# Kernel tuning notes

Measured on AMD Instinct MI355X. Metric: run time of the kernel, lower is better.

The kernel has to match this reference:

```python
import jax, jax.numpy as jnp
import numpy as np

B, P, C = 256, 196, 512       # batch, num_pixels, encoder_dim
D, A, E = 512, 256, 256       # decoder_dim, attention_dim, embedding_dim
V, TC = 193, 256              # vocab, caption length (decode steps = TC-1)


def _lin(k, out_d, in_d):
    s = 1.0 / np.sqrt(in_d)
    return jax.random.uniform(k, (out_d, in_d), jnp.float32, -s, s)


def setup_inputs() -> dict:
    key = jax.random.key(0)
    ks = jax.random.split(key, 16)
    lens = jax.random.randint(ks[1], (B,), 2, TC + 1).at[0].set(TC)
    inp = {
        "encoder_output": jax.random.normal(ks[0], (B, P, C), jnp.float32),
        "encoded_captions": jax.random.randint(ks[2], (B, TC), 0, V),
        "caption_lengths": lens[:, None],
        # attention
        "W_enc_att": _lin(ks[3], A, C), "b_enc_att": jnp.zeros((A,), jnp.float32),
        "W_dec_att": _lin(ks[4], A, D), "b_dec_att": jnp.zeros((A,), jnp.float32),
        "W_full_att": _lin(ks[5], 1, A), "b_full_att": jnp.zeros((1,), jnp.float32),
        # embedding (init uniform(-0.1, 0.1) as in init_weigths)
        "embedding": jax.random.uniform(ks[6], (V, E), jnp.float32, -0.1, 0.1),
        # output projection
        "W_fc": jax.random.uniform(ks[7], (V, D), jnp.float32, -0.1, 0.1),
        "b_fc": jnp.zeros((V,), jnp.float32),
        # LSTMCell: input is [emb ; attended_enc] -> E + C
        "W_ih": _lin(ks[8], 4 * D, E + C), "b_ih": jnp.zeros((4 * D,), jnp.float32),
        "W_hh": _lin(ks[9], 4 * D, D), "b_hh": jnp.zeros((4 * D,), jnp.float32),
        # hidden/cell init + gate
        "W_init_h": _lin(ks[10], D, C), "b_init_h": jnp.zeros((D,), jnp.float32),
        "W_init_c": _lin(ks[11], D, C), "b_init_c": jnp.zeros((D,), jnp.float32),
        "W_fbeta": _lin(ks[12], D, C), "b_fbeta": jnp.zeros((D,), jnp.float32),
    }
    return inp


def reference(encoder_output, encoded_captions, caption_lengths,
              W_enc_att, b_enc_att, W_dec_att, b_dec_att, W_full_att, b_full_att,
              embedding, W_fc, b_fc, W_ih, b_ih, W_hh, b_hh,
              W_init_h, b_init_h, W_init_c, b_init_c, W_fbeta, b_fbeta):
    b = encoder_output.shape[0]
    enc = encoder_output.reshape(b, -1, encoder_output.shape[-1])  # [B,P,C]
    lens = caption_lengths[:, 0]
    sort_index = jnp.argsort(-lens)                 # descending length sort
    lens = lens[sort_index]
    enc = enc[sort_index]
    caps = encoded_captions[sort_index]
    decode_lengths = lens - 1
    T = caps.shape[1] - 1                           # static max decode steps

    embs = embedding[caps]                          # [B,TC,E]
    mean_enc = enc.mean(axis=1)                     # [B,C]
    h0 = mean_enc @ W_init_h.T + b_init_h
    c0 = mean_enc @ W_init_c.T + b_init_c

    enc_att = enc @ W_enc_att.T + b_enc_att         # [B,P,A] precomputed
    wf, bf = W_full_att[0], b_full_att[0]

    def step(carry, xs):
        h, c = carry
        emb_t, t = xs
        # soft attention
        dec_att = h @ W_dec_att.T + b_dec_att                       # [B,A]
        scores = jnp.einsum('bpa,a->bp',
                            jax.nn.relu(enc_att + dec_att[:, None, :]), wf) + bf
        alpha = jax.nn.softmax(scores, axis=1)                      # [B,P]
        awe = jnp.einsum('bpc,bp->bc', enc, alpha)                  # [B,C]
        gate = jax.nn.sigmoid(h @ W_fbeta.T + b_fbeta)              # [B,D]
        awe = gate * awe
        # LSTM cell (torch gate order: i,f,g,o); dropout is identity in eval
        x = jnp.concatenate([emb_t, awe], axis=1)                   # [B,E+C]
        gates = x @ W_ih.T + b_ih + h @ W_hh.T + b_hh
        i_g, f_g, g_g, o_g = jnp.split(gates, 4, axis=1)
        c_new = jax.nn.sigmoid(f_g) * c + jax.nn.sigmoid(i_g) * jnp.tanh(g_g)
        h_new = jax.nn.sigmoid(o_g) * jnp.tanh(c_new)
        # shrinking-batch semantics: inactive rows keep state, emit zeros
        active = (t < decode_lengths)[:, None]
        h2 = jnp.where(active, h_new, h)
        c2 = jnp.where(active, c_new, c)
        preds = jnp.where(active, h_new @ W_fc.T + b_fc, 0.0)
        alpha = jnp.where(active, alpha, 0.0)
        return (h2, c2), (preds, alpha)

    xs = (jnp.swapaxes(embs[:, :T], 0, 1), jnp.arange(T))
    _, (preds, alphas) = jax.lax.scan(step, (h0, c0), xs)
    predictions = jnp.swapaxes(preds, 0, 1)   # [B,T,V]
    alphas = jnp.swapaxes(alphas, 0, 1)       # [B,T,P]
    return predictions, caps, decode_lengths, alphas, sort_index
```

## Files before the change

kernel.cpp:

```cpp
#include <hip/hip_runtime.h>
#include <cstdint>
#include <cstddef>


typedef unsigned short u16;
typedef unsigned int u32;
typedef unsigned long long ull;
typedef __attribute__((ext_vector_type(8))) short short8;
typedef __attribute__((ext_vector_type(4))) float f32x4;

__device__ __forceinline__ float sigf(float x){ return 1.f/(1.f+expf(-x)); }
__device__ __forceinline__ u16 f2bf(float f){
  u32 u = __builtin_bit_cast(u32, f);
  u32 r = (u + 0x7fffu + ((u>>16)&1u)) >> 16;
  return (u16)r;
}
__device__ __forceinline__ float bf2f(u16 u){
  u32 x = ((u32)u) << 16;
  return __builtin_bit_cast(float, x);
}

__device__ __forceinline__ void st_dev_f32(float* p, float v){
  __hip_atomic_store(p, v, __ATOMIC_RELAXED, __HIP_MEMORY_SCOPE_AGENT);
}
__device__ __forceinline__ float ld_dev_f32(const float* p){
  return __hip_atomic_load(p, __ATOMIC_RELAXED, __HIP_MEMORY_SCOPE_AGENT);
}
__device__ __forceinline__ void st_dev_u16(u16* p, u16 v){
  __hip_atomic_store(p, v, __ATOMIC_RELAXED, __HIP_MEMORY_SCOPE_AGENT);
}
__device__ __forceinline__ void st_dev_u32(u32* p, u32 v){
  __hip_atomic_store(p, v, __ATOMIC_RELAXED, __HIP_MEMORY_SCOPE_AGENT);
}
__device__ __forceinline__ u32 ld_dev_u32(const u32* p){
  return __hip_atomic_load(p, __ATOMIC_RELAXED, __HIP_MEMORY_SCOPE_AGENT);
}
__device__ __forceinline__ ull ld_dev_u64(const ull* p){
  return __hip_atomic_load(p, __ATOMIC_RELAXED, __HIP_MEMORY_SCOPE_AGENT);
}

__device__ __forceinline__ void ctr_signal(int* c){
  __syncthreads();
  if (threadIdx.x == 0)
    __hip_atomic_fetch_add(c, 1, __ATOMIC_RELAXED, __HIP_MEMORY_SCOPE_AGENT);
}
__device__ __forceinline__ void ctr_wait(int* c, int target){
  if (threadIdx.x == 0){
    int spins = 0;
    while (__hip_atomic_load(c, __ATOMIC_RELAXED, __HIP_MEMORY_SCOPE_AGENT) < target){
      if (++spins > (1<<20)) break;
      __builtin_amdgcn_s_sleep(4);
    }
  }
  __syncthreads();
}

__global__ void k_zero(float* a, int na4, float* b, int nb4, int* ctr){
  int i = blockIdx.x*blockDim.x + threadIdx.x;
  int stride = gridDim.x*blockDim.x;
  float4 z = make_float4(0.f,0.f,0.f,0.f);
  for (int j = i; j < na4; j += stride) ((float4*)a)[j] = z;
  for (int j = i; j < nb4; j += stride) ((float4*)b)[j] = z;
  if (i < 512) ctr[i] = 0;
}

__global__ void k_sort(const int* cap_lens, int* si, int* dlw, float* out_dl, float* out_si){
  __shared__ int lens[256];
  int tid = threadIdx.x;
  lens[tid] = cap_lens[tid];
  __syncthreads();
  int L = lens[tid];
  int rank = 0;
  for (int j = 0; j < 256; ++j){
    int Lj = lens[j];
    rank += ((Lj > L) || (Lj == L && j < tid)) ? 1 : 0;
  }
  si[rank] = tid;
  dlw[rank] = L - 1;
  out_dl[rank] = (float)(L - 1);
  out_si[rank] = (float)tid;
}

__global__ void k_caps(const int* caps, const int* si, int* caps_s, float* out_caps){
  int b = blockIdx.x, t = threadIdx.x;
  int v = caps[si[b]*256 + t];
  caps_s[b*256 + t] = v;
  out_caps[b*256 + t] = (float)v;
}

__global__ void k_prep(const float* enc, const int* si, u16* enc_sb){
  int b = blockIdx.x, tid = threadIdx.x;
  const float* src = enc + (size_t)si[b]*100352;
  u16* dst = enc_sb + (size_t)b*100352;
  for (int i = tid; i < 25088; i += 256){
    float4 v = *(const float4*)&src[i*4];
    ushort4 o;
    o.x = f2bf(v.x); o.y = f2bf(v.y); o.z = f2bf(v.z); o.w = f2bf(v.w);
    *(ushort4*)&dst[i*4] = o;
  }
}

__global__ void k_mean(const float* enc, const int* si, u16* mean_bf){
  int b = blockIdx.x, tid = threadIdx.x;
  const float* eb = enc + (size_t)si[b]*100352;
  int cc = 2*tid;
  float s0 = 0.f, s1 = 0.f;
  #pragma unroll 4
  for (int pp = 0; pp < 196; ++pp){
    float2 v = *(const float2*)&eb[(size_t)pp*512 + cc];
    s0 += v.x; s1 += v.y;
  }
  mean_bf[b*512 + cc]     = f2bf(s0 * (1.f/196.f));
  mean_bf[b*512 + cc + 1] = f2bf(s1 * (1.f/196.f));
}

struct ConcatP {
  const float *Wdec,*bdec,*Wfb,*bfb,*Wfc,*bfc,*Wih,*bih,*Whh,*bhh,*Winh,*binh,*Winc,*binc,*Wenc,*emb;
  u16 *Wc0,*Wc1,*Wc3,*Wenc_bf,*emb_bf;
  float *bc0,*bc1,*bc3;
};
__global__ void k_concat(ConcatP p){
  int idx = blockIdx.x*blockDim.x + threadIdx.x;
  int stride = gridDim.x*blockDim.x;
  for (int i = idx; i < 1024*512; i += stride){
    int n = i >> 9, k = i & 511;
    float v = (n < 512) ? p.Winh[n*512 + k] : p.Winc[(n-512)*512 + k];
    p.Wc0[i] = f2bf(v);
  }
  for (int i = idx; i < 1024; i += stride)
    p.bc0[i] = (i < 512) ? p.binh[i] : p.binc[i-512];
  for (int i = idx; i < 1024*512; i += stride){
    int n = i >> 9, k = i & 511;
    float v = (n < 256) ? p.Wdec[n*512+k]
            : (n < 768) ? p.Wfb[(n-256)*512+k]
            : (n < 961) ? p.Wfc[(n-768)*512+k] : 0.f;
    p.Wc1[i] = f2bf(v);
  }
  for (int i = idx; i < 1024; i += stride)
    p.bc1[i] = (i < 256) ? p.bdec[i] : (i < 768) ? p.bfb[i-256] : (i < 961) ? p.bfc[i-768] : 0.f;
  for (int i = idx; i < 2048*1280; i += stride){
    int n = i / 1280, k = i - n*1280;
    int j = n >> 2, g = n & 3, orow = g*512 + j;
    float v = (k < 768) ? p.Wih[orow*768 + k] : p.Whh[orow*512 + (k - 768)];
    p.Wc3[i] = f2bf(v);
  }
  for (int i = idx; i < 2048; i += stride){
    int j = i >> 2, g = i & 3, orow = g*512 + j;
    p.bc3[i] = p.bih[orow] + p.bhh[orow];
  }
  for (int i = idx; i < 256*512; i += stride) p.Wenc_bf[i] = f2bf(p.Wenc[i]);
  for (int i = idx; i < 193*256; i += stride) p.emb_bf[i] = f2bf(p.emb[i]);
}

struct MfmaP {
  const u16* A; const u16* Bw; const float* bias;
  int K, N;
  u16* out_bf;
  u16* h_bf; float* c;
};

template<int MODE, int NT>
__global__ __launch_bounds__(256) void k_mfma(MfmaP p){
  __shared__ __align__(16) unsigned char smem[16384 + 16384*NT];
  u16* As0 = (u16*)smem;
  u16* Bs0 = (u16*)(smem + 16384);

  const int tid  = threadIdx.x;
  const int bn0  = blockIdx.x * 64 * NT;
  const int bm0  = blockIdx.y * 64;
  const int wave = tid >> 6;
  const int lane = tid & 63;
  const int ln   = lane & 15;
  const int quad = lane >> 4;

  f32x4 acc[4][NT] = {};
  short8 pa[2], pb[2*NT];

  const int srow = tid >> 3;
  const int sgc  = tid & 7;

  #pragma unroll
  for (int r = 0; r < 2; ++r)
    pa[r] = *(const short8*)(p.A + (size_t)(bm0 + srow + 32*r)*p.K + sgc*8);
  #pragma unroll
  for (int r = 0; r < 2*NT; ++r)
    pb[r] = *(const short8*)(p.Bw + (size_t)(bn0 + srow + 32*r)*p.K + sgc*8);
  #pragma unroll
  for (int r = 0; r < 2; ++r){
    int row = srow + 32*r;
    *(short8*)&As0[row*64 + ((sgc ^ (row & 7))<<3)] = pa[r];
  }
  #pragma unroll
  for (int r = 0; r < 2*NT; ++r){
    int row = srow + 32*r;
    *(short8*)&Bs0[row*64 + ((sgc ^ (row & 7))<<3)] = pb[r];
  }

  const int nIter = p.K >> 6;
  int ib = 0;
  for (int it = 0; ; ){
    __syncthreads();
    const bool more = (it + 1 < nIter);
    if (more){
      int k0 = (it + 1) << 6;
      #pragma unroll
      for (int r = 0; r < 2; ++r)
        pa[r] = *(const short8*)(p.A + (size_t)(bm0 + srow + 32*r)*p.K + k0 + sgc*8);
      #pragma unroll
      for (int r = 0; r < 2*NT; ++r)
        pb[r] = *(const short8*)(p.Bw + (size_t)(bn0 + srow + 32*r)*p.K + k0 + sgc*8);
    }
    const u16* As = &As0[ib*4096];
    const u16* Bs = &Bs0[ib*4096*NT];
    #pragma unroll
    for (int kk = 0; kk < 2; ++kk){
      short8 af[4], bfr[NT];
      #pragma unroll
      for (int mt = 0; mt < 4; ++mt){
        int row = mt*16 + ln;
        int g = kk*4 + quad;
        af[mt] = *(const short8*)&As[row*64 + ((g ^ (row & 7))<<3)];
      }
      #pragma unroll
      for (int nt = 0; nt < NT; ++nt){
        int row = (wave*NT + nt)*16 + ln;
        int g = kk*4 + quad;
        bfr[nt] = *(const short8*)&Bs[row*64 + ((g ^ (row & 7))<<3)];
      }
      #pragma unroll
      for (int mt = 0; mt < 4; ++mt)
        #pragma unroll
        for (int nt = 0; nt < NT; ++nt)
          acc[mt][nt] = __builtin_amdgcn_mfma_f32_16x16x32_bf16(af[mt], bfr[nt], acc[mt][nt], 0, 0, 0);
    }
    if (!more) break;
    ib ^= 1;
    u16* Aw = &As0[ib*4096];
    u16* Bww = &Bs0[ib*4096*NT];
    #pragma unroll
    for (int r = 0; r < 2; ++r){
      int row = srow + 32*r;
      *(short8*)&Aw[row*64 + ((sgc ^ (row & 7))<<3)] = pa[r];
    }
    #pragma unroll
    for (int r = 0; r < 2*NT; ++r){
      int row = srow + 32*r;
      *(short8*)&Bww[row*64 + ((sgc ^ (row & 7))<<3)] = pb[r];
    }
    ++it;
  }

  #pragma unroll
  for (int nt = 0; nt < NT; ++nt){
    int n = bn0 + (wave*NT + nt)*16 + ln;
    float bv = p.bias[n];
    #pragma unroll
    for (int mt = 0; mt < 4; ++mt)
      #pragma unroll
      for (int r = 0; r < 4; ++r){
        int m = bm0 + mt*16 + quad*4 + r;
        float v = acc[mt][nt][r] + bv;
        if (MODE == 0){
          p.out_bf[(size_t)m*p.N + n] = f2bf(v);
        } else {
          if (n < 512) p.h_bf[m*512 + n] = f2bf(v);
          else         p.c[m*512 + n - 512] = v;
        }
      }
  }
}

struct PersistP {
  const u16* Wc1; const float* bc1;
  const u16* Wc3; const float* bc3;
  u16* h_bf; float* c; u16* z_bf;
  float* dec_att; float* gatev; float* preds; float* alphas;
  const u16* enc_att; const u16* enc_sb;
  const float* wfull; const float* bfull;
  const u16* emb_bf; const int* caps_s;
  const int* dl;
  int* ctr;
};

template<int NC, int MODE>
__device__ void gemm_phase(const PersistP& p, unsigned char* smem, int bm0, int bn0, int t){
  constexpr int K = NC * 64;
  constexpr int DP = (NC < 4) ? NC : 4;
  const u16* A    = (MODE == 2) ? p.h_bf : p.z_bf;
  const u16* Bw   = (MODE == 2) ? p.Wc1  : p.Wc3;
  const float* bias = (MODE == 2) ? p.bc1 : p.bc3;

  const int tid = threadIdx.x;
  const int w = tid >> 6, l = tid & 63;
  const int half = tid >> 9;
  const int loc = tid & 511;
  const int r = loc >> 3, g = loc & 7;
  u16* lds0 = (u16*)smem;
  u16* ldst = lds0 + (half ? 4096 : 0) + r*64 + ((g ^ (r & 7)) << 3);
  const u16* gp = half ? (Bw + (size_t)(bn0 + r)*K + g*8)
                       : (A  + (size_t)(bm0 + r)*K + g*8);
  const int mt = w >> 2, nt = w & 3;
  const int ln = l & 15, quad = l >> 4;
  f32x4 acc = {0.f,0.f,0.f,0.f};

  ull buf[DP][2];
  auto issue = [&](int ci, int slot){
    const u16* q = gp + ci*64;
    if (half == 0){
      buf[slot][0] = ld_dev_u64((const ull*)q);
      buf[slot][1] = ld_dev_u64((const ull*)q + 1);
    } else {
      buf[slot][0] = ((const ull*)q)[0];
      buf[slot][1] = ((const ull*)q)[1];
    }
  };
  auto wr = [&](int ci, int slot){
    u16* d = ldst + (ci & 1)*8192;
    ((ull*)d)[0] = buf[slot][0];
    ((ull*)d)[1] = buf[slot][1];
  };
  auto compute = [&](int ci){
    const u16* As = lds0 + (ci & 1)*8192;
    const u16* Bs = As + 4096;
    #pragma unroll
    for (int kk = 0; kk < 2; ++kk){
      int gg = kk*4 + quad;
      int ra = mt*16 + ln;
      short8 af = *(const short8*)&As[ra*64 + ((gg ^ (ra & 7))<<3)];
      int rb = nt*16 + ln;
      short8 bv = *(const short8*)&Bs[rb*64 + ((gg ^ (rb & 7))<<3)];
      acc = __builtin_amdgcn_mfma_f32_16x16x32_bf16(af, bv, acc, 0, 0, 0);
    }
  };

  #pragma unroll
  for (int s = 0; s < DP; ++s) issue(s, s);
  wr(0, 0);
  asm volatile("s_waitcnt lgkmcnt(0)" ::: "memory");
  __builtin_amdgcn_s_barrier();
  #pragma unroll
  for (int ci = 0; ci < NC; ++ci){
    if (ci + 1 < NC) wr(ci + 1, (ci + 1) % DP);
    if (ci + DP < NC) issue(ci + DP, (ci + DP) % DP);
    compute(ci);
    asm volatile("s_waitcnt lgkmcnt(0)" ::: "memory");
    __builtin_amdgcn_s_barrier();
  }

  if (MODE == 2){
    const int n = bn0 + nt*16 + ln;
    const float bv = bias[n];
    #pragma unroll
    for (int rr = 0; rr < 4; ++rr){
      int m = bm0 + mt*16 + quad*4 + rr;
      float v = acc[rr] + bv;
      if (n < 256)      st_dev_f32(&p.dec_att[m*256 + n], v);
      else if (n < 768) st_dev_f32(&p.gatev[m*512 + n - 256], sigf(v));
      else if (n < 961){
        int tp = t - 1;
        if (tp >= 0)
          p.preds[((size_t)m*255 + tp)*193 + (n - 768)] = (tp < p.dl[m]) ? v : 0.f;
      }
    }
  } else {
    float* Cs = (float*)smem;
    const int n_loc = nt*16 + ln;
    const float bv = bias[bn0 + n_loc];
    __syncthreads();
    #pragma unroll
    for (int rr = 0; rr < 4; ++rr)
      Cs[(mt*16 + quad*4 + rr)*68 + n_loc] = acc[rr] + bv;
    __syncthreads();
    {
      int m = tid >> 4, jl = tid & 15;
      float4 g4 = *(const float4*)&Cs[m*68 + jl*4];
      int gm = bm0 + m;
      int gj = (bn0 >> 2) + jl;
      if (t < p.dl[gm]){
        float ig = sigf(g4.x), fg = sigf(g4.y);
        float gg = tanhf(g4.z), og = sigf(g4.w);
        float cn = fg * p.c[gm*512 + gj] + ig * gg;
        float hn = og * tanhf(cn);
        p.c[gm*512 + gj] = cn;
        st_dev_u16(&p.h_bf[gm*512 + gj], f2bf(hn));
      }
    }
  }
}

__device__ void attn_phase(const PersistP& p, unsigned char* smem_raw, int b, int t){
  float* da  = (float*)smem_raw;
  float* wfs = da + 256;
  float* sc  = wfs + 256;
  float* awe = sc + 256;
  float* red = awe + 2048;
  const int tid = threadIdx.x;
  if (tid < 256){
    da[tid]  = ld_dev_f32(&p.dec_att[b*256 + tid]);
    wfs[tid] = p.wfull[tid];
  }
  __syncthreads();

  {
    const int pr = tid >> 2, aq = tid & 3;
    float s = 0.f;
    if (pr < 196){
      const u16* row = p.enc_att + ((size_t)b*196 + pr)*256 + aq*64;
      const float* dd = &da[aq*64];
      const float* ww = &wfs[aq*64];
      #pragma unroll
      for (int i = 0; i < 8; ++i){
        short8 v = *(const short8*)(row + i*8);
        #pragma unroll
        for (int j = 0; j < 8; ++j)
          s += fmaxf(bf2f((u16)v[j]) + dd[i*8+j], 0.f) * ww[i*8+j];
      }
    }
    s += __shfl_xor(s, 1, 64);
    s += __shfl_xor(s, 2, 64);
    if ((tid & 3) == 0 && pr < 196) sc[pr] = s + p.bfull[0];
  }
  __syncthreads();

  const int wid = tid >> 6, lane = tid & 63;
  float sv = (tid < 196) ? sc[tid] : -1e30f;
  float mx = sv;
  for (int o = 32; o > 0; o >>= 1) mx = fmaxf(mx, __shfl_down(mx, o, 64));
  if (lane == 0) red[wid] = mx;
  __syncthreads();
  if (tid == 0) red[16] = fmaxf(fmaxf(red[0], red[1]), fmaxf(red[2], red[3]));
  __syncthreads();
  mx = red[16];
  float e = (tid < 196) ? expf(sv - mx) : 0.f;
  float sm = e;
  for (int o = 32; o > 0; o >>= 1) sm += __shfl_down(sm, o, 64);
  if (lane == 0) red[wid] = sm;
  __syncthreads();
  if (tid == 0) red[16] = red[0] + red[1] + red[2] + red[3];
  __syncthreads();
  const float inv = 1.f / red[16];
  if (tid < 256) sc[tid] = e * inv;
  __syncthreads();
  if (tid < 196)
    p.alphas[((size_t)b*255 + t)*196 + tid] = sc[tid];

  {
    const int q = tid >> 8, cp = tid & 255, cc = 2*cp;
    const u16* eb = p.enc_sb + (size_t)b*100352;
    const int p0 = q*49;
    float v0 = 0.f, v1 = 0.f;
    #pragma unroll 7
    for (int i = 0; i < 49; ++i){
      int pp = p0 + i;
      u32 u = *(const u32*)&eb[(size_t)pp*512 + cc];
      float a = sc[pp];
      v0 += a * bf2f((u16)(u & 0xffffu));
      v1 += a * bf2f((u16)(u >> 16));
    }
    *(float2*)&awe[q*512 + cc] = make_float2(v0, v1);
  }
  __syncthreads();

  if (tid < 256){
    const int cc = 2*tid;
    float v0 = awe[0*512+cc]   + awe[1*512+cc]   + awe[2*512+cc]   + awe[3*512+cc];
    float v1 = awe[0*512+cc+1] + awe[1*512+cc+1] + awe[2*512+cc+1] + awe[3*512+cc+1];
    u16* zb = p.z_bf + (size_t)b*1280;
    float g0 = ld_dev_f32(&p.gatev[b*512 + cc]);
    float g1 = ld_dev_f32(&p.gatev[b*512 + cc + 1]);
    st_dev_u16(&zb[256 + cc],     f2bf(g0 * v0));
    st_dev_u16(&zb[256 + cc + 1], f2bf(g1 * v1));
    int tok = p.caps_s[b*256 + t];
    st_dev_u16(&zb[tid], p.emb_bf[tok*256 + tid]);
    st_dev_u32((u32*)&zb[768 + cc], ld_dev_u32((const u32*)&p.h_bf[b*512 + cc]));
  }
}

__global__ __launch_bounds__(1024) void k_persist(PersistP p){
  __shared__ __align__(16) unsigned char smem[40960];
  const int b = blockIdx.x;
  for (int t = 0; t <= 255; ++t){
    if (b >= 192){
      const int idx = b - 192, x = idx & 15, y = idx >> 4;
      ctr_wait(p.ctr + 256 + y*32, 32*t);
      if (p.dl[y*64] >= t)
        gemm_phase<8,2>(p, smem, y*64, x*64, t);
      ctr_signal(p.ctr + 0 + y*32);
    }
    if (t == 255) break;
    {
      const int y = b >> 6;
      ctr_wait(p.ctr + 0 + y*32, 16*(t+1));
      if (t < p.dl[b]) attn_phase(p, smem, b, t);
      ctr_signal(p.ctr + 128 + y*32);
    }
    if (b < 128){
      const int x = b & 31, y = b >> 5;
      ctr_wait(p.ctr + 128 + y*32, 64*(t+1));
      if (p.dl[y*64] > t)
        gemm_phase<20,3>(p, smem, y*64, x*64, t);
      ctr_signal(p.ctr + 256 + y*32);
    }
  }
}

extern "C" void kernel_launch(void* const* d_in, const int* in_sizes, int n_in,
                              void* d_out, int out_size, void* d_ws, size_t ws_size,
                              hipStream_t stream){
  (void)in_sizes; (void)n_in; (void)out_size; (void)ws_size;
  const float* enc   = (const float*)d_in[0];
  const int*   caps  = (const int*)d_in[1];
  const int*   clens = (const int*)d_in[2];
  const float* Wenc  = (const float*)d_in[3];
  const float* benc  = (const float*)d_in[4];
  const float* Wdec  = (const float*)d_in[5];
  const float* bdec  = (const float*)d_in[6];
  const float* Wfull = (const float*)d_in[7];
  const float* bfull = (const float*)d_in[8];
  const float* emb   = (const float*)d_in[9];
  const float* Wfc   = (const float*)d_in[10];
  const float* bfc   = (const float*)d_in[11];
  const float* Wih   = (const float*)d_in[12];
  const float* bih   = (const float*)d_in[13];
  const float* Whh   = (const float*)d_in[14];
  const float* bhh   = (const float*)d_in[15];
  const float* Winh  = (const float*)d_in[16];
  const float* binh  = (const float*)d_in[17];
  const float* Winc  = (const float*)d_in[18];
  const float* binc  = (const float*)d_in[19];
  const float* Wfb   = (const float*)d_in[20];
  const float* bfb   = (const float*)d_in[21];

  float* out       = (float*)d_out;
  float* out_preds = out;
  float* out_caps  = out + 12599040;
  float* out_dl    = out + 12664576;
  float* out_alph  = out + 12664832;
  float* out_si    = out + 25459712;

  char* w = (char*)d_ws;
  size_t off = 0;
  auto alloc = [&](size_t bytes) -> void* {
    void* pp = w + off; off += (bytes + 255) & ~(size_t)255; return pp;
  };
  int*   si      = (int*)  alloc(256*4);
  int*   dlw     = (int*)  alloc(256*4);
  int*   caps_s  = (int*)  alloc(65536*4);
  float* c       = (float*)alloc(131072*4);
  float* dec_att = (float*)alloc(65536*4);
  float* gatev   = (float*)alloc(131072*4);
  float* bc0     = (float*)alloc(1024*4);
  float* bc1     = (float*)alloc(1024*4);
  float* bc3     = (float*)alloc(2048*4);
  int*   ctr     = (int*)  alloc(1024*4);
  u16*   mean_bf = (u16*)  alloc(131072*2);
  u16*   h_bf    = (u16*)  alloc(131072*2);
  u16*   z_bf    = (u16*)  alloc(327680*2);
  u16*   Wc0     = (u16*)  alloc(524288*2);
  u16*   Wc1     = (u16*)  alloc(524288*2);
  u16*   Wc3     = (u16*)  alloc(2621440*2);
  u16*   Wenc_bf = (u16*)  alloc(131072*2);
  u16*   emb_bf  = (u16*)  alloc(49408*2);
  u16*   enc_sb  = (u16*)  alloc(25690112ull*2);
  u16*   enc_att = (u16*)  alloc(12845056ull*2);

  k_zero<<<1024, 256, 0, stream>>>(out_preds, 12599040/4, out_alph, 12794880/4, ctr);
  k_sort<<<1, 256, 0, stream>>>(clens, si, dlw, out_dl, out_si);
  k_caps<<<256, 256, 0, stream>>>(caps, si, caps_s, out_caps);
  k_prep<<<256, 256, 0, stream>>>(enc, si, enc_sb);
  k_mean<<<256, 256, 0, stream>>>(enc, si, mean_bf);
  ConcatP cp{Wdec,bdec,Wfb,bfb,Wfc,bfc,Wih,bih,Whh,bhh,Winh,binh,Winc,binc,Wenc,emb,
             Wc0,Wc1,Wc3,Wenc_bf,emb_bf,bc0,bc1,bc3};
  k_concat<<<2048, 256, 0, stream>>>(cp);

  {
    MfmaP g{};
    g.A = mean_bf; g.Bw = Wc0; g.bias = bc0; g.K = 512; g.N = 1024;
    g.h_bf = h_bf; g.c = c;
    k_mfma<1,1><<<dim3(16,4), 256, 0, stream>>>(g);
  }
  {
    MfmaP g{};
    g.A = enc_sb; g.Bw = Wenc_bf; g.bias = benc; g.K = 512; g.N = 256;
    g.out_bf = enc_att;
    k_mfma<0,2><<<dim3(2,784), 256, 0, stream>>>(g);
  }

  PersistP pp{};
  pp.Wc1 = Wc1; pp.bc1 = bc1; pp.Wc3 = Wc3; pp.bc3 = bc3;
  pp.h_bf = h_bf; pp.c = c; pp.z_bf = z_bf;
  pp.dec_att = dec_att; pp.gatev = gatev; pp.preds = out_preds; pp.alphas = out_alph;
  pp.enc_att = enc_att; pp.enc_sb = enc_sb;
  pp.wfull = Wfull; pp.bfull = bfull;
  pp.emb_bf = emb_bf; pp.caps_s = caps_s;
  pp.dl = dlw; pp.ctr = ctr;

  void* kargs[] = { (void*)&pp };
  hipError_t e = hipLaunchCooperativeKernel((const void*)k_persist, dim3(256), dim3(1024),
                                            kargs, 0, stream);
  if (e != hipSuccess){
    k_persist<<<dim3(256), dim3(1024), 0, stream>>>(pp);
  }
}
```

Measured before the change: 8.351 ms.

## Replace atomic counters with per-block flags and finer-grained dependency waits

Swaps the shared atomic-increment counters between persistent phases for per-producer flag slots that each block stores with the step number. Waiters poll all flags with one wavefront using a wave-wide all-reduce. The attention phase now waits only on the first four gate-GEMM tiles (the dec_att columns) before starting, and waits on the remaining gate tiles just before it needs gatev. This cuts atomic contention and overlaps attention work with the rest of that GEMM, but it depends on the tile-to-column mapping being right and on the inactive-row paths still storing their flags.

```diff
diff --git a/kernel.cpp b/kernel.cpp
--- a/kernel.cpp
+++ b/kernel.cpp
@@ -39,17 +39,21 @@
   return __hip_atomic_load(p, __ATOMIC_RELAXED, __HIP_MEMORY_SCOPE_AGENT);
 }
 
-__device__ __forceinline__ void ctr_signal(int* c){
+__device__ __forceinline__ void flag_store(int* f, int v){
   __syncthreads();
   if (threadIdx.x == 0)
-    __hip_atomic_fetch_add(c, 1, __ATOMIC_RELAXED, __HIP_MEMORY_SCOPE_AGENT);
-}
-__device__ __forceinline__ void ctr_wait(int* c, int target){
-  if (threadIdx.x == 0){
+    __hip_atomic_store(f, v, __ATOMIC_RELAXED, __HIP_MEMORY_SCOPE_AGENT);
+}
+__device__ __forceinline__ void flags_wait(const int* f, int n, int target){
+  if (threadIdx.x < 64){
+    const int lane = threadIdx.x;
     int spins = 0;
-    while (__hip_atomic_load(c, __ATOMIC_RELAXED, __HIP_MEMORY_SCOPE_AGENT) < target){
+    for (;;){
+      int v = (lane < n) ? __hip_atomic_load(&f[lane], __ATOMIC_RELAXED, __HIP_MEMORY_SCOPE_AGENT)
+                         : 0x7fffffff;
+      if (__all(v >= target)) break;
       if (++spins > (1<<20)) break;
-      __builtin_amdgcn_s_sleep(4);
+      __builtin_amdgcn_s_sleep(2);
     }
   }
   __syncthreads();
@@ -388,7 +392,8 @@
   }
 }
 
-__device__ void attn_phase(const PersistP& p, unsigned char* smem_raw, int b, int t){
+__device__ void attn_phase(const PersistP& p, unsigned char* smem_raw, int b, int t,
+                           const int* f_gate, int target){
   float* da  = (float*)smem_raw;
   float* wfs = da + 256;
   float* sc  = wfs + 256;
@@ -459,7 +464,8 @@
     }
     *(float2*)&awe[q*512 + cc] = make_float2(v0, v1);
   }
-  __syncthreads();
+
+  flags_wait(f_gate, 8, target);
 
   if (tid < 256){
     const int cc = 2*tid;
@@ -479,27 +485,32 @@
 __global__ __launch_bounds__(1024) void k_persist(PersistP p){
   __shared__ __align__(16) unsigned char smem[40960];
   const int b = blockIdx.x;
+  int* f1 = p.ctr;
+  int* f2 = p.ctr + 64;
+  int* f3 = p.ctr + 320;
   for (int t = 0; t <= 255; ++t){
     if (b >= 192){
       const int idx = b - 192, x = idx & 15, y = idx >> 4;
-      ctr_wait(p.ctr + 256 + y*32, 32*t);
+      flags_wait(f3 + y*32, 32, t);
       if (p.dl[y*64] >= t)
         gemm_phase<8,2>(p, smem, y*64, x*64, t);
-      ctr_signal(p.ctr + 0 + y*32);
+      flag_store(&f1[y*16 + x], t + 1);
     }
     if (t == 255) break;
     {
       const int y = b >> 6;
-      ctr_wait(p.ctr + 0 + y*32, 16*(t+1));
-      if (t < p.dl[b]) attn_phase(p, smem, b, t);
-      ctr_signal(p.ctr + 128 + y*32);
+      if (t < p.dl[b]){
+        flags_wait(f1 + y*16, 4, t + 1);
+        attn_phase(p, smem, b, t, f1 + y*16 + 4, t + 1);
+      }
+      flag_store(&f2[b], t + 1);
     }
     if (b < 128){
       const int x = b & 31, y = b >> 5;
-      ctr_wait(p.ctr + 128 + y*32, 64*(t+1));
+      flags_wait(f2 + y*64, 64, t + 1);
       if (p.dl[y*64] > t)
         gemm_phase<20,3>(p, smem, y*64, x*64, t);
-      ctr_signal(p.ctr + 256 + y*32);
+      flag_store(&f3[y*32 + x], t + 1);
     }
   }
 }
```

Result: faster. 8.167 ms (-2.2%).
